# Optimization experiments

Hardware: AMD Instinct MI355X
Metric: run time of the kernel (lower is better)

## Reference

```python
import jax, jax.numpy as jnp
import numpy as np

B, N, D_IN, D_OUT = 16, 2048, 128, 128

def setup_inputs() -> dict:
    key = jax.random.key(0)
    ks = jax.random.split(key, 8)
    x = jax.random.normal(ks[0], (B, N, D_IN), dtype=jnp.float32)
    adj = jax.random.randint(ks[1], (N, N), 0, 2).astype(jnp.float32)
    # Conv1d(kernel_size=1) weights, PyTorch default uniform init scale
    s_emb = 1.0 / np.sqrt(D_IN)
    W_emb = jax.random.uniform(ks[2], (D_OUT, D_IN), jnp.float32, -s_emb, s_emb)
    b_emb = jax.random.uniform(ks[3], (D_OUT,), jnp.float32, -s_emb, s_emb)
    s_qk = 1.0 / np.sqrt(D_OUT)
    w_q = jax.random.uniform(ks[4], (D_OUT,), jnp.float32, -s_qk, s_qk)
    b_q = jax.random.uniform(ks[5], (1,), jnp.float32, -s_qk, s_qk)
    w_k = jax.random.uniform(ks[6], (D_OUT,), jnp.float32, -s_qk, s_qk)
    b_k = jax.random.uniform(ks[7], (1,), jnp.float32, -s_qk, s_qk)
    return {"x": x, "adj": adj, "W_emb": W_emb, "b_emb": b_emb,
            "w_q": w_q, "b_q": b_q, "w_k": w_k, "b_k": b_k}

def reference(x, adj, W_emb, b_emb, w_q, b_q, w_k, b_k):
    # emb_conv: 1x1 conv over node dim == per-node linear  [B,N,D_out]
    seq_fts = jnp.einsum('bni,oi->bno', x, W_emb) + b_emb
    # q_conv / k_conv: project to scalar per node  [B,N]
    q = jnp.einsum('bnd,d->bn', seq_fts, w_q) + b_q  # f_1_t squeezed
    k = jnp.einsum('bnd,d->bn', seq_fts, w_k) + b_k  # f_2_t squeezed
    # f[b,i,j] = f_1_t[b,0,j] + f_2_t^T[b,i,0] = q[b,j] + k[b,i]
    f = k[:, :, None] + q[:, None, :]                 # [B,N,N]
    f = jax.nn.leaky_relu(adj[None, :, :] * f, negative_slope=0.01)
    coefs = jax.nn.softmax(f, axis=1)                 # softmax over dim=1 (rows)
    vals = jnp.einsum('bij,bjd->bid', coefs, seq_fts)  # [B,N,D_out]
    return vals
```

## Files before the change

### kernel.cpp

```cpp
#include <hip/hip_runtime.h>
#include <hip/hip_bf16.h>
#include <stdint.h>

#define B_ 16
#define N_ 2048
#define D_ 128

typedef __bf16 bf16_t;
typedef bf16_t bf16x8 __attribute__((ext_vector_type(8)));
typedef float f32x4 __attribute__((ext_vector_type(4)));

__global__ __launch_bounds__(256) void k_pack_adj(const float* __restrict__ adj,
                                                  unsigned int* __restrict__ bits) {
    int t = blockIdx.x * 256 + threadIdx.x;
    float v = adj[t];
    unsigned long long m = __ballot(v > 0.5f);
    if ((t & 63) == 0) {
        int i = t >> 11;
        int j = t & 2047;
        bits[i * 64 + (j >> 5)]     = (unsigned int)m;
        bits[i * 64 + (j >> 5) + 1] = (unsigned int)(m >> 32);
    }
}

__global__ __launch_bounds__(256, 2) void k_emb(const float* __restrict__ x,
                                                const float* __restrict__ W,
                                                const float* __restrict__ be,
                                                const float* __restrict__ wq,
                                                const float* __restrict__ bq,
                                                const float* __restrict__ wk,
                                                const float* __restrict__ bk,
                                                bf16_t* __restrict__ Pb,
                                                float* __restrict__ qa, float* __restrict__ ka,
                                                float* __restrict__ Eq, float* __restrict__ eqs,
                                                float* __restrict__ Ek, float* __restrict__ eks) {
    __shared__ float xs[32][68];
    __shared__ float ws[32][132];
    __shared__ float qs[64], ks[64];
    int b  = blockIdx.y;
    int n0 = blockIdx.x * 64;
    int tid = threadIdx.x;
    int tx = tid & 15, ty = tid >> 4;
    if (tid < 64) { qs[tid] = 0.f; ks[tid] = 0.f; }

    float acc[4][8] = {};
    f32x4 xr[2], wr[4];

    auto loadregs = [&](int kc) {
#pragma unroll
        for (int s = 0; s < 2; ++s) {
            int p = tid + 256 * s;
            int n = p >> 3, kq = p & 7;
            xr[s] = *(const f32x4*)(x + ((size_t)(b * N_ + n0 + n)) * D_ + kc * 32 + kq * 4);
        }
#pragma unroll
        for (int s = 0; s < 4; ++s) {
            int p = tid + 256 * s;
            int d = p >> 3, kq = p & 7;
            wr[s] = *(const f32x4*)(W + (size_t)d * D_ + kc * 32 + kq * 4);
        }
    };
    auto writelds = [&]() {
#pragma unroll
        for (int s = 0; s < 2; ++s) {
            int p = tid + 256 * s;
            int n = p >> 3, kq = p & 7;
#pragma unroll
            for (int u = 0; u < 4; ++u) xs[kq * 4 + u][n] = xr[s][u];
        }
#pragma unroll
        for (int s = 0; s < 4; ++s) {
            int p = tid + 256 * s;
            int d = p >> 3, kq = p & 7;
#pragma unroll
            for (int u = 0; u < 4; ++u) ws[kq * 4 + u][d] = wr[s][u];
        }
    };

    loadregs(0);
    for (int kc = 0; kc < 4; ++kc) {
        writelds();
        __syncthreads();
        if (kc < 3) loadregs(kc + 1);
#pragma unroll 4
        for (int k = 0; k < 32; ++k) {
            f32x4 xv  = *(const f32x4*)&xs[k][tx * 4];
            f32x4 wv0 = *(const f32x4*)&ws[k][ty * 8];
            f32x4 wv1 = *(const f32x4*)&ws[k][ty * 8 + 4];
#pragma unroll
            for (int i = 0; i < 4; ++i)
#pragma unroll
                for (int j = 0; j < 8; ++j)
                    acc[i][j] += xv[i] * ((j < 4) ? wv0[j] : wv1[j - 4]);
        }
        __syncthreads();
    }

    float qp[4] = {}, kp[4] = {};
#pragma unroll
    for (int j = 0; j < 8; ++j) {
        int d = ty * 8 + j;
        float bj  = be[d];
        float wqj = wq[d];
        float wkj = wk[d];
        f32x4 o;
        bf16_t ob[4];
#pragma unroll
        for (int i = 0; i < 4; ++i) {
            o[i] = acc[i][j] + bj;
            qp[i] += o[i] * wqj;
            kp[i] += o[i] * wkj;
            ob[i] = (bf16_t)o[i];
        }
        *(uint2*)(Pb + ((size_t)b * D_ + d) * N_ + n0 + tx * 4) = *(uint2*)ob;
    }
#pragma unroll
    for (int i = 0; i < 4; ++i) {
        atomicAdd(&qs[tx * 4 + i], qp[i]);
        atomicAdd(&ks[tx * 4 + i], kp[i]);
    }
    __syncthreads();
    if (tid < 64) {
        int idx = b * N_ + n0 + tid;
        float aq = qs[tid] + bq[0];
        float ak = ks[tid] + bk[0];
        qa[idx] = aq;          ka[idx] = ak;
        Eq[idx] = expf(aq);    eqs[idx] = expf(0.01f * aq);
        Ek[idx] = expf(ak);    eks[idx] = expf(0.01f * ak);
    }
}

__global__ __launch_bounds__(256) void k_denom(const unsigned int* __restrict__ bits,
                                               const float* __restrict__ qa,
                                               const float* __restrict__ ka,
                                               const float* __restrict__ Eq,
                                               const float* __restrict__ eqs,
                                               const float* __restrict__ Ek,
                                               const float* __restrict__ eks,
                                               float* __restrict__ denom) {
    int jt  = blockIdx.x;
    int b   = blockIdx.y;
    int seg = blockIdx.z;
    int j = jt * 256 + threadIdx.x;
    float qj  = qa[b * N_ + j];
    float Eqj = Eq[b * N_ + j];
    float eqj = eqs[b * N_ + j];
    int shift = j & 31;
    int wid   = j >> 5;
    float acc = 0.f;
    int i0 = seg * 256;
#pragma unroll 16
    for (int i = i0; i < i0 + 256; ++i) {
        float kk  = ka[b * N_ + i];
        float Ekk = Ek[b * N_ + i];
        float ekk = eks[b * N_ + i];
        unsigned int w = bits[i * 64 + wid];
        float z  = kk + qj;
        float f1 = z > 0.f ? Ekk : ekk;
        float f2 = z > 0.f ? Eqj : eqj;
        float v  = f1 * f2;
        acc += ((w >> shift) & 1u) ? v : 1.0f;
    }
    atomicAdd(&denom[b * N_ + j], acc);
}

__global__ __launch_bounds__(256, 2) void k_attn(const float* __restrict__ Eq,
                                                 const float* __restrict__ eqs,
                                                 const float* __restrict__ Ek,
                                                 const float* __restrict__ eks,
                                                 const float* __restrict__ denom,
                                                 const unsigned int* __restrict__ bits,
                                                 const bf16_t* __restrict__ Pb,
                                                 float* __restrict__ out) {
    __shared__ __align__(16) bf16_t ldsB[2][128 * 64];
    int b     = blockIdx.y;
    int ibase = blockIdx.x * 64;
    int tid   = threadIdx.x;
    int w     = tid >> 6;
    int lane  = tid & 63;
    int m16   = lane & 15;
    int quad  = lane >> 4;
    int ig    = w & 1;
    int dg    = w >> 1;

    int iA = ibase + (2 * ig) * 16 + m16;
    int iB = iA + 16;
    float EkR0 = Ek[b * N_ + iA],  EkR1 = Ek[b * N_ + iB];
    float ekR0 = eks[b * N_ + iA], ekR1 = eks[b * N_ + iB];
    float TR0 = __builtin_amdgcn_rcpf(EkR0);
    float TR1 = __builtin_amdgcn_rcpf(EkR1);
    const unsigned int* brA = bits + (size_t)iA * 64;
    const unsigned int* brB = bits + (size_t)iB * 64;
    const float* Eqp = Eq    + b * N_;
    const float* eqp = eqs   + b * N_;
    const float* dnp = denom + b * N_;
    const bf16_t* PtB = Pb + (size_t)b * D_ * N_;

    f32x4 acc[2][4];
#pragma unroll
    for (int c = 0; c < 2; ++c)
#pragma unroll
        for (int nt = 0; nt < 4; ++nt) acc[c][nt] = (f32x4){0.f, 0.f, 0.f, 0.f};

    f32x4 Ev[2][2][2], ev[2][2][2], dv[2][2][2];
    uint2 mA[2], mB[2];

    auto ldj = [&](int par, int jb) {
#pragma unroll
        for (int hh = 0; hh < 2; ++hh) {
            int j0 = jb + hh * 32 + quad * 8;
            Ev[par][hh][0] = *(const f32x4*)(Eqp + j0);
            Ev[par][hh][1] = *(const f32x4*)(Eqp + j0 + 4);
            ev[par][hh][0] = *(const f32x4*)(eqp + j0);
            ev[par][hh][1] = *(const f32x4*)(eqp + j0 + 4);
            dv[par][hh][0] = *(const f32x4*)(dnp + j0);
            dv[par][hh][1] = *(const f32x4*)(dnp + j0 + 4);
        }
        mA[par] = *(const uint2*)&brA[jb >> 5];
        mB[par] = *(const uint2*)&brB[jb >> 5];
    };

    auto stage = [&](int bufi, int jb) {
#pragma unroll
        for (int t = 0; t < 4; ++t) {
            int off = t * 4096 + tid * 16;
            int d   = off >> 7;
            int g   = ((off & 127) >> 4) ^ (d & 7);
            const bf16_t* gp = PtB + (size_t)d * N_ + jb + g * 8;
            __builtin_amdgcn_global_load_lds(
                (const __attribute__((address_space(1))) void*)gp,
                (__attribute__((address_space(3))) void*)((char*)(&ldsB[bufi][0]) + off),
                16, 0, 0);
        }
    };

    stage(0, 0);
    ldj(0, 0);
    __syncthreads();
    int buf = 0;
#pragma unroll 1
    for (int s2 = 0; s2 < N_ / 128; ++s2) {
#pragma unroll
        for (int par = 0; par < 2; ++par) {
            int step = s2 * 2 + par;
            int jb = step * 64;
            if (step + 1 < N_ / 64) {
                stage(buf ^ 1, jb + 64);
                ldj(par ^ 1, jb + 64);
            }

            bf16x8 af[2][2];
#pragma unroll
            for (int hh = 0; hh < 2; ++hh) {
                unsigned int wdA = hh ? mA[par].y : mA[par].x;
                unsigned int wdB = hh ? mB[par].y : mB[par].x;
#pragma unroll
                for (int t = 0; t < 8; ++t) {
                    float Eqj = (t < 4) ? Ev[par][hh][0][t] : Ev[par][hh][1][t - 4];
                    float eqj = (t < 4) ? ev[par][hh][0][t] : ev[par][hh][1][t - 4];
                    float dj  = (t < 4) ? dv[par][hh][0][t] : dv[par][hh][1][t - 4];
                    float rdj = __builtin_amdgcn_rcpf(dj);
                    int bit = quad * 8 + t;
                    {
                        bool c = Eqj > TR0;
                        float v = (c ? EkR0 : ekR0) * (c ? Eqj : eqj) * rdj;
                        af[0][hh][t] = (bf16_t)(((wdA >> bit) & 1u) ? v : rdj);
                    }
                    {
                        bool c = Eqj > TR1;
                        float v = (c ? EkR1 : ekR1) * (c ? Eqj : eqj) * rdj;
                        af[1][hh][t] = (bf16_t)(((wdB >> bit) & 1u) ? v : rdj);
                    }
                }
            }

#pragma unroll
            for (int hh = 0; hh < 2; ++hh) {
                int cph = ((hh * 4 + quad) ^ (m16 & 7)) * 8;
#pragma unroll
                for (int nt = 0; nt < 4; ++nt) {
                    int d = dg * 64 + nt * 16 + m16;
                    bf16x8 bf = *(const bf16x8*)&ldsB[buf][d * 64 + cph];
                    acc[0][nt] = __builtin_amdgcn_mfma_f32_16x16x32_bf16(af[0][hh], bf, acc[0][nt], 0, 0, 0);
                    acc[1][nt] = __builtin_amdgcn_mfma_f32_16x16x32_bf16(af[1][hh], bf, acc[1][nt], 0, 0, 0);
                }
            }
            __syncthreads();
            buf ^= 1;
        }
    }

#pragma unroll
    for (int c = 0; c < 2; ++c) {
        int irow = ibase + (2 * ig + c) * 16 + quad * 4;
#pragma unroll
        for (int nt = 0; nt < 4; ++nt) {
            int d = dg * 64 + nt * 16 + m16;
#pragma unroll
            for (int r = 0; r < 4; ++r)
                out[((size_t)b * N_ + irow + r) * D_ + d] = acc[c][nt][r];
        }
    }
}

extern "C" void kernel_launch(void* const* d_in, const int* in_sizes, int n_in,
                              void* d_out, int out_size, void* d_ws, size_t ws_size,
                              hipStream_t stream) {
    const float* x   = (const float*)d_in[0];
    const float* adj = (const float*)d_in[1];
    const float* W   = (const float*)d_in[2];
    const float* be  = (const float*)d_in[3];
    const float* wq  = (const float*)d_in[4];
    const float* bq  = (const float*)d_in[5];
    const float* wk  = (const float*)d_in[6];
    const float* bk  = (const float*)d_in[7];
    float* out = (float*)d_out;

    char* ws = (char*)d_ws;
    size_t off = 0;
    bf16_t* Pb = (bf16_t*)(ws + off); off += (size_t)B_ * D_ * N_ * 2;
    float* qa  = (float*)(ws + off);  off += (size_t)B_ * N_ * 4;
    float* ka  = (float*)(ws + off);  off += (size_t)B_ * N_ * 4;
    float* denom = (float*)(ws + off); off += (size_t)B_ * N_ * 4;
    float* Eq  = (float*)(ws + off);  off += (size_t)B_ * N_ * 4;
    float* eqs = (float*)(ws + off);  off += (size_t)B_ * N_ * 4;
    float* Ek  = (float*)(ws + off);  off += (size_t)B_ * N_ * 4;
    float* eks = (float*)(ws + off);  off += (size_t)B_ * N_ * 4;
    unsigned int* bits = (unsigned int*)(ws + off); off += (size_t)N_ * 64 * 4;

    hipMemsetAsync(denom, 0, (size_t)B_ * N_ * 4, stream);

    k_pack_adj<<<N_ * N_ / 256, 256, 0, stream>>>(adj, bits);
    k_emb<<<dim3(N_ / 64, B_), 256, 0, stream>>>(x, W, be, wq, bq, wk, bk,
                                                 Pb, qa, ka, Eq, eqs, Ek, eks);
    k_denom<<<dim3(8, 16, 8), 256, 0, stream>>>(bits, qa, ka, Eq, eqs, Ek, eks, denom);
    k_attn<<<dim3(N_ / 64, B_), 256, 0, stream>>>(Eq, eqs, Ek, eks, denom, bits, Pb, out);
}
```

Before: 208.3 us.

## Share attention-weight computation across waves via LDS and precompute reciprocal denominators

Each wave pair previously built the full A fragment (both 32-column halves) redundantly; now each wave computes only its half of the column block and exchanges it through a small LDS buffer with an extra barrier. A new elementwise kernel precomputes 1/denom and folds it into Eq and eqs, removing per-element reciprocal and a multiply from the inner loop, and the sign test now compares q against -k directly. This halves the VALU exp-weight work in k_attn at the cost of an extra launch, extra LDS traffic and a barrier per step.

```diff
diff --git a/kernel.cpp b/kernel.cpp
--- a/kernel.cpp
+++ b/kernel.cpp
@@ -164,15 +164,31 @@
     atomicAdd(&denom[b * N_ + j], acc);
 }
 
-__global__ __launch_bounds__(256, 2) void k_attn(const float* __restrict__ Eq,
-                                                 const float* __restrict__ eqs,
+__global__ __launch_bounds__(256) void k_post(const float* __restrict__ denom,
+                                              const float* __restrict__ Eq,
+                                              const float* __restrict__ eqs,
+                                              float* __restrict__ rd,
+                                              float* __restrict__ Eqr,
+                                              float* __restrict__ eqr) {
+    int t = blockIdx.x * 256 + threadIdx.x;
+    float r = 1.0f / denom[t];
+    rd[t]  = r;
+    Eqr[t] = Eq[t] * r;
+    eqr[t] = eqs[t] * r;
+}
+
+__global__ __launch_bounds__(256, 2) void k_attn(const float* __restrict__ qa,
+                                                 const float* __restrict__ ka,
                                                  const float* __restrict__ Ek,
                                                  const float* __restrict__ eks,
-                                                 const float* __restrict__ denom,
+                                                 const float* __restrict__ rd,
+                                                 const float* __restrict__ Eqr,
+                                                 const float* __restrict__ eqr,
                                                  const unsigned int* __restrict__ bits,
                                                  const bf16_t* __restrict__ Pb,
                                                  float* __restrict__ out) {
     __shared__ __align__(16) bf16_t ldsB[2][128 * 64];
+    __shared__ __align__(16) bf16_t ldsA[4 * 2 * 64 * 8];
     int b     = blockIdx.y;
     int ibase = blockIdx.x * 64;
     int tid   = threadIdx.x;
@@ -185,15 +201,15 @@
 
     int iA = ibase + (2 * ig) * 16 + m16;
     int iB = iA + 16;
+    float mkR0 = -ka[b * N_ + iA], mkR1 = -ka[b * N_ + iB];
     float EkR0 = Ek[b * N_ + iA],  EkR1 = Ek[b * N_ + iB];
     float ekR0 = eks[b * N_ + iA], ekR1 = eks[b * N_ + iB];
-    float TR0 = __builtin_amdgcn_rcpf(EkR0);
-    float TR1 = __builtin_amdgcn_rcpf(EkR1);
     const unsigned int* brA = bits + (size_t)iA * 64;
     const unsigned int* brB = bits + (size_t)iB * 64;
-    const float* Eqp = Eq    + b * N_;
-    const float* eqp = eqs   + b * N_;
-    const float* dnp = denom + b * N_;
+    const float* qp  = qa  + b * N_;
+    const float* Erp = Eqr + b * N_;
+    const float* erp = eqr + b * N_;
+    const float* rdp = rd  + b * N_;
     const bf16_t* PtB = Pb + (size_t)b * D_ * N_;
 
     f32x4 acc[2][4];
@@ -202,22 +218,21 @@
 #pragma unroll
         for (int nt = 0; nt < 4; ++nt) acc[c][nt] = (f32x4){0.f, 0.f, 0.f, 0.f};
 
-    f32x4 Ev[2][2][2], ev[2][2][2], dv[2][2][2];
-    uint2 mA[2], mB[2];
+    f32x4 qv4[2][2], Er4[2][2], er4[2][2], rd4[2][2];
+    unsigned int mA[2], mB[2];
 
     auto ldj = [&](int par, int jb) {
-#pragma unroll
-        for (int hh = 0; hh < 2; ++hh) {
-            int j0 = jb + hh * 32 + quad * 8;
-            Ev[par][hh][0] = *(const f32x4*)(Eqp + j0);
-            Ev[par][hh][1] = *(const f32x4*)(Eqp + j0 + 4);
-            ev[par][hh][0] = *(const f32x4*)(eqp + j0);
-            ev[par][hh][1] = *(const f32x4*)(eqp + j0 + 4);
-            dv[par][hh][0] = *(const f32x4*)(dnp + j0);
-            dv[par][hh][1] = *(const f32x4*)(dnp + j0 + 4);
-        }
-        mA[par] = *(const uint2*)&brA[jb >> 5];
-        mB[par] = *(const uint2*)&brB[jb >> 5];
+        int j0 = jb + dg * 32 + quad * 8;
+        qv4[par][0] = *(const f32x4*)(qp  + j0);
+        qv4[par][1] = *(const f32x4*)(qp  + j0 + 4);
+        Er4[par][0] = *(const f32x4*)(Erp + j0);
+        Er4[par][1] = *(const f32x4*)(Erp + j0 + 4);
+        er4[par][0] = *(const f32x4*)(erp + j0);
+        er4[par][1] = *(const f32x4*)(erp + j0 + 4);
+        rd4[par][0] = *(const f32x4*)(rdp + j0);
+        rd4[par][1] = *(const f32x4*)(rdp + j0 + 4);
+        mA[par] = brA[(jb >> 5) + dg];
+        mB[par] = brB[(jb >> 5) + dg];
     };
 
     auto stage = [&](int bufi, int jb) {
@@ -245,44 +260,55 @@
             int step = s2 * 2 + par;
             int jb = step * 64;
             if (step + 1 < N_ / 64) {
+                ldj(par ^ 1, jb + 64);
                 stage(buf ^ 1, jb + 64);
-                ldj(par ^ 1, jb + 64);
             }
 
-            bf16x8 af[2][2];
-#pragma unroll
-            for (int hh = 0; hh < 2; ++hh) {
-                unsigned int wdA = hh ? mA[par].y : mA[par].x;
-                unsigned int wdB = hh ? mB[par].y : mB[par].x;
-#pragma unroll
-                for (int t = 0; t < 8; ++t) {
-                    float Eqj = (t < 4) ? Ev[par][hh][0][t] : Ev[par][hh][1][t - 4];
-                    float eqj = (t < 4) ? ev[par][hh][0][t] : ev[par][hh][1][t - 4];
-                    float dj  = (t < 4) ? dv[par][hh][0][t] : dv[par][hh][1][t - 4];
-                    float rdj = __builtin_amdgcn_rcpf(dj);
-                    int bit = quad * 8 + t;
-                    {
-                        bool c = Eqj > TR0;
-                        float v = (c ? EkR0 : ekR0) * (c ? Eqj : eqj) * rdj;
-                        af[0][hh][t] = (bf16_t)(((wdA >> bit) & 1u) ? v : rdj);
-                    }
-                    {
-                        bool c = Eqj > TR1;
-                        float v = (c ? EkR1 : ekR1) * (c ? Eqj : eqj) * rdj;
-                        af[1][hh][t] = (bf16_t)(((wdB >> bit) & 1u) ? v : rdj);
-                    }
+            bf16x8 afA, afB;
+#pragma unroll
+            for (int t = 0; t < 8; ++t) {
+                float qv = (t < 4) ? qv4[par][0][t] : qv4[par][1][t - 4];
+                float Er = (t < 4) ? Er4[par][0][t] : Er4[par][1][t - 4];
+                float er = (t < 4) ? er4[par][0][t] : er4[par][1][t - 4];
+                float rj = (t < 4) ? rd4[par][0][t] : rd4[par][1][t - 4];
+                int bit = quad * 8 + t;
+                {
+                    bool c = qv > mkR0;
+                    float v = (c ? EkR0 : ekR0) * (c ? Er : er);
+                    afA[t] = (bf16_t)(((mA[par] >> bit) & 1u) ? v : rj);
+                }
+                {
+                    bool c = qv > mkR1;
+                    float v = (c ? EkR1 : ekR1) * (c ? Er : er);
+                    afB[t] = (bf16_t)(((mB[par] >> bit) & 1u) ? v : rj);
                 }
             }
-
-#pragma unroll
-            for (int hh = 0; hh < 2; ++hh) {
-                int cph = ((hh * 4 + quad) ^ (m16 & 7)) * 8;
+            *(bf16x8*)((char*)ldsA + ((((2 * ig + 0) * 2 + dg) * 64 + lane) * 16)) = afA;
+            *(bf16x8*)((char*)ldsA + ((((2 * ig + 1) * 2 + dg) * 64 + lane) * 16)) = afB;
+
+            asm volatile("s_waitcnt lgkmcnt(0)\n\ts_barrier" ::: "memory");
+
+            {
+                int cph = ((dg * 4 + quad) ^ (m16 & 7)) * 8;
 #pragma unroll
                 for (int nt = 0; nt < 4; ++nt) {
                     int d = dg * 64 + nt * 16 + m16;
                     bf16x8 bf = *(const bf16x8*)&ldsB[buf][d * 64 + cph];
-                    acc[0][nt] = __builtin_amdgcn_mfma_f32_16x16x32_bf16(af[0][hh], bf, acc[0][nt], 0, 0, 0);
-                    acc[1][nt] = __builtin_amdgcn_mfma_f32_16x16x32_bf16(af[1][hh], bf, acc[1][nt], 0, 0, 0);
+                    acc[0][nt] = __builtin_amdgcn_mfma_f32_16x16x32_bf16(afA, bf, acc[0][nt], 0, 0, 0);
+                    acc[1][nt] = __builtin_amdgcn_mfma_f32_16x16x32_bf16(afB, bf, acc[1][nt], 0, 0, 0);
+                }
+            }
+            {
+                int oh = 1 - dg;
+                bf16x8 a0 = *(const bf16x8*)((char*)ldsA + ((((2 * ig + 0) * 2 + oh) * 64 + lane) * 16));
+                bf16x8 a1 = *(const bf16x8*)((char*)ldsA + ((((2 * ig + 1) * 2 + oh) * 64 + lane) * 16));
+                int cph = ((oh * 4 + quad) ^ (m16 & 7)) * 8;
+#pragma unroll
+                for (int nt = 0; nt < 4; ++nt) {
+                    int d = dg * 64 + nt * 16 + m16;
+                    bf16x8 bf = *(const bf16x8*)&ldsB[buf][d * 64 + cph];
+                    acc[0][nt] = __builtin_amdgcn_mfma_f32_16x16x32_bf16(a0, bf, acc[0][nt], 0, 0, 0);
+                    acc[1][nt] = __builtin_amdgcn_mfma_f32_16x16x32_bf16(a1, bf, acc[1][nt], 0, 0, 0);
                 }
             }
             __syncthreads();
@@ -326,6 +352,9 @@
     float* eqs = (float*)(ws + off);  off += (size_t)B_ * N_ * 4;
     float* Ek  = (float*)(ws + off);  off += (size_t)B_ * N_ * 4;
     float* eks = (float*)(ws + off);  off += (size_t)B_ * N_ * 4;
+    float* rd  = (float*)(ws + off);  off += (size_t)B_ * N_ * 4;
+    float* Eqr = (float*)(ws + off);  off += (size_t)B_ * N_ * 4;
+    float* eqr = (float*)(ws + off);  off += (size_t)B_ * N_ * 4;
     unsigned int* bits = (unsigned int*)(ws + off); off += (size_t)N_ * 64 * 4;
 
     hipMemsetAsync(denom, 0, (size_t)B_ * N_ * 4, stream);
@@ -334,5 +363,7 @@
     k_emb<<<dim3(N_ / 64, B_), 256, 0, stream>>>(x, W, be, wq, bq, wk, bk,
                                                  Pb, qa, ka, Eq, eqs, Ek, eks);
     k_denom<<<dim3(8, 16, 8), 256, 0, stream>>>(bits, qa, ka, Eq, eqs, Ek, eks, denom);
-    k_attn<<<dim3(N_ / 64, B_), 256, 0, stream>>>(Eq, eqs, Ek, eks, denom, bits, Pb, out);
-}
+    k_post<<<B_ * N_ / 256, 256, 0, stream>>>(denom, Eq, eqs, rd, Eqr, eqr);
+    k_attn<<<dim3(N_ / 64, B_), 256, 0, stream>>>(qa, ka, Ek, eks, rd, Eqr, eqr,
+                                                  bits, Pb, out);
+}
```

Result: faster. 187.1 us (-10.2%).
